# Kernel optimization log

Hardware: AMD Instinct MI355X
Metric: run time of the kernel (lower is better)

## Reference

```python
import jax, jax.numpy as jnp
import numpy as np

BETA = 0.25

def _l2norm(x, eps=1e-12):
    # F.normalize(x, dim=-1)
    n = jnp.sqrt(jnp.sum(x * x, axis=-1, keepdims=True))
    return x / jnp.maximum(n, eps)

def setup_inputs() -> dict:
    key = jax.random.key(0)
    k1, k2 = jax.random.split(key)
    z = jax.random.normal(k1, (32, 1024, 32), dtype=jnp.float32)
    embedding = jax.random.normal(k2, (8192, 32), dtype=jnp.float32)
    return {"z": z, "embedding": embedding}

def reference(z, embedding):
    B, T, D = z.shape
    zf = _l2norm(z.reshape(-1, D))            # [N, D]
    en = _l2norm(embedding)                   # [n_e, D]
    # squared distances: ||z||^2 + ||e||^2 - 2 z.e  -> [N, n_e]
    d = (jnp.sum(zf * zf, axis=1, keepdims=True)
         + jnp.sum(en * en, axis=1)
         - 2.0 * jnp.einsum('nd,kd->nk', zf, en))
    idx = jnp.argmin(d, axis=1).reshape(B, T)            # [B, T]
    z_q = embedding[idx]                                  # [B, T, D] gather
    z_qnorm = _l2norm(z_q)
    z_norm = _l2norm(z)
    loss = (BETA * jnp.mean((jax.lax.stop_gradient(z_qnorm) - z_norm) ** 2)
            + jnp.mean((z_qnorm - jax.lax.stop_gradient(z_norm)) ** 2))
    # straight-through estimator
    z_q_out = z + jax.lax.stop_gradient(z_qnorm - z)
    return z_q_out, loss, idx
```

## Files before the change

kernel.cpp:

```cpp
#include <hip/hip_runtime.h>
#include <math.h>


#define D 32
#define KCODES 8192
#define MARGIN 2.5e-4f
#define EPS 1e-12f

typedef short bf16x8 __attribute__((ext_vector_type(8)));
typedef unsigned short u16x8 __attribute__((ext_vector_type(8)));
typedef float f32x4 __attribute__((ext_vector_type(4)));

static __device__ __forceinline__ unsigned short f2bf(float x) {
  unsigned u = __float_as_uint(x);
  return (unsigned short)((u + 0x7FFFu + ((u >> 16) & 1u)) >> 16);
}
static __device__ __forceinline__ float bf2f(unsigned short s) {
  return __uint_as_float(((unsigned)s) << 16);
}
static __device__ __forceinline__ void gload_lds16(const void* g, void* l) {
  __builtin_amdgcn_global_load_lds(
      (const __attribute__((address_space(1))) void*)g,
      (__attribute__((address_space(3))) void*)l, 16, 0, 0);
}


__global__ __launch_bounds__(256) void k_prep(const float* __restrict__ z,
                                              const float* __restrict__ emb,
                                              float* __restrict__ en,
                                              float* __restrict__ en_h,
                                              unsigned short* __restrict__ eswz,
                                              unsigned short* __restrict__ zswz_hi,
                                              unsigned short* __restrict__ zswz_lo,
                                              float* __restrict__ zn,
                                              int* __restrict__ cnt,
                                              float* __restrict__ loss,
                                              unsigned long long* __restrict__ mp2,
                                              int N) {
  int v = blockIdx.x * 256 + threadIdx.x;
  if (v == 0) { *cnt = 0; *loss = 0.f; }
  if (v >= KCODES + N) return;
  if (v >= KCODES) mp2[v - KCODES] = 0ull;
  const float* src = (v < KCODES) ? (emb + (size_t)v * D) : (z + (size_t)(v - KCODES) * D);

  float x[D];
  const float4* p = reinterpret_cast<const float4*>(src);
#pragma unroll
  for (int j = 0; j < D / 4; ++j) {
    float4 q = p[j];
    x[4 * j + 0] = q.x; x[4 * j + 1] = q.y; x[4 * j + 2] = q.z; x[4 * j + 3] = q.w;
  }
  float ss = 0.f;
#pragma unroll
  for (int j = 0; j < D; ++j) ss = fmaf(x[j], x[j], ss);
  float n = fmaxf(sqrtf(ss), EPS);
#pragma unroll
  for (int j = 0; j < D; ++j) x[j] = x[j] / n;

  unsigned short hi[D], lo[D];
#pragma unroll
  for (int j = 0; j < D; ++j) {
    hi[j] = f2bf(x[j]);
    lo[j] = f2bf(x[j] - bf2f(hi[j]));
  }

  if (v < KCODES) {
    float4* o = reinterpret_cast<float4*>(en + (size_t)v * D);
    float s2 = 0.f;
#pragma unroll
    for (int j = 0; j < D / 4; ++j) {
      float4 q = {x[4 * j], x[4 * j + 1], x[4 * j + 2], x[4 * j + 3]};
      s2 = fmaf(q.x, q.x, fmaf(q.y, q.y, fmaf(q.z, q.z, fmaf(q.w, q.w, s2))));
      o[j] = q;
    }
    en_h[v] = 0.5f * s2;
    int tl = v >> 4, m = v & 15;
#pragma unroll
    for (int q = 0; q < 4; ++q) {
      u16x8 hv, lv;
#pragma unroll
      for (int j = 0; j < 8; ++j) { hv[j] = hi[8 * q + j]; lv[j] = lo[8 * q + j]; }
      *(u16x8*)(eswz + (size_t)tl * 1024 + (q * 16 + m) * 8) = hv;
      *(u16x8*)(eswz + (size_t)tl * 1024 + 512 + (q * 16 + m) * 8) = lv;
    }
  } else {
    int r = v - KCODES;
    float4* zo = reinterpret_cast<float4*>(zn + (size_t)r * D);
#pragma unroll
    for (int j = 0; j < D / 4; ++j) {
      float4 q = {x[4 * j], x[4 * j + 1], x[4 * j + 2], x[4 * j + 3]};
      zo[j] = q;
    }
    int g = r >> 4, m = r & 15;
#pragma unroll
    for (int q = 0; q < 4; ++q) {
      u16x8 hv, lv;
#pragma unroll
      for (int j = 0; j < 8; ++j) { hv[j] = hi[8 * q + j]; lv[j] = lo[8 * q + j]; }
      *(u16x8*)(zswz_hi + (size_t)g * 512 + (q * 16 + m) * 8) = hv;
      *(u16x8*)(zswz_lo + (size_t)g * 512 + (q * 16 + m) * 8) = lv;
    }
  }
}

__global__ __launch_bounds__(256, 2) void k_argmin_mfma(
    const unsigned short* __restrict__ zswz_hi,
    const unsigned short* __restrict__ zswz_lo,
    const unsigned short* __restrict__ eswz,
    float* __restrict__ res_s1, int* __restrict__ res_cb,
    float* __restrict__ res_s2) {
  __shared__ unsigned short lds_sh[2][16384];

  const int tid = threadIdx.x;
  const int wid = tid >> 6, lane = tid & 63;
  const int lane15 = lane & 15, quad = lane >> 4;
  const int rs = blockIdx.x >> 2;
  const int qt = blockIdx.x & 3;

  bf16x8 zhi[4], zlo[4];
#pragma unroll
  for (int rg = 0; rg < 4; ++rg) {
    int g = rs * 16 + wid * 4 + rg;
    zhi[rg] = *(const bf16x8*)(zswz_hi + (size_t)g * 512 + lane * 8);
    zlo[rg] = *(const bf16x8*)(zswz_lo + (size_t)g * 512 + lane * 8);
  }

  float cm[4], s1g[4], s2c[4];
  int cb[4];
#pragma unroll
  for (int rg = 0; rg < 4; ++rg) {
    cm[rg] = -3.4e38f; s1g[rg] = -3.4e38f; s2c[rg] = -3.4e38f; cb[rg] = 0;
  }
  const f32x4 zero4 = {0.f, 0.f, 0.f, 0.f};

  const float4* gall = reinterpret_cast<const float4*>(eswz) + (size_t)qt * 8 * 2048;
#pragma unroll
  for (int i = 0; i < 8; ++i) {
    int off = i * 256 + tid;
    gload_lds16(gall + off, (char*)&lds_sh[0][0] + (size_t)off * 16);
  }

  for (int c = 0; c < 8; ++c) {
    __syncthreads();
    if (c + 1 < 8) {
      const float4* gn = gall + (size_t)(c + 1) * 2048;
      char* dst = (char*)&lds_sh[(c + 1) & 1][0];
#pragma unroll
      for (int i = 0; i < 8; ++i) {
        int off = i * 256 + tid;
        gload_lds16(gn + off, dst + (size_t)off * 16);
      }
    }
    const unsigned short* buf = &lds_sh[c & 1][0];
#pragma unroll
    for (int t = 0; t < 16; ++t) {
      bf16x8 ahi = *(const bf16x8*)(buf + t * 1024 + lane * 8);
      bf16x8 alo = *(const bf16x8*)(buf + t * 1024 + 512 + lane * 8);
#pragma unroll
      for (int rg = 0; rg < 4; ++rg) {
        f32x4 acc = __builtin_amdgcn_mfma_f32_16x16x32_bf16(ahi, zhi[rg], zero4, 0, 0, 0);
        acc = __builtin_amdgcn_mfma_f32_16x16x32_bf16(ahi, zlo[rg], acc, 0, 0, 0);
        acc = __builtin_amdgcn_mfma_f32_16x16x32_bf16(alo, zhi[rg], acc, 0, 0, 0);
        cm[rg] = fmaxf(cm[rg],
                       fmaxf(fmaxf(acc[0], acc[1]), fmaxf(acc[2], acc[3])));
      }
    }
#pragma unroll
    for (int rg = 0; rg < 4; ++rg) {
      float old1 = s1g[rg];
      s2c[rg] = fmaxf(s2c[rg], fminf(cm[rg], old1));
      bool better = cm[rg] > old1;
      cb[rg] = better ? (qt * 8 + c) : cb[rg];
      s1g[rg] = better ? cm[rg] : old1;
      cm[rg] = -3.4e38f;
    }
  }

#pragma unroll
  for (int m = 16; m <= 32; m <<= 1) {
#pragma unroll
    for (int rg = 0; rg < 4; ++rg) {
      float o1 = __shfl_xor(s1g[rg], m, 64);
      float o2 = __shfl_xor(s2c[rg], m, 64);
      int ob = __shfl_xor(cb[rg], m, 64);
      s2c[rg] = fmaxf(fmaxf(s2c[rg], o2), fminf(s1g[rg], o1));
      bool better = o1 > s1g[rg];
      s1g[rg] = better ? o1 : s1g[rg];
      cb[rg] = better ? ob : cb[rg];
    }
  }
  if (quad == 0) {
#pragma unroll
    for (int rg = 0; rg < 4; ++rg) {
      int row = rs * 256 + wid * 64 + rg * 16 + lane15;
      res_s1[(size_t)row * 4 + qt] = s1g[rg];
      res_cb[(size_t)row * 4 + qt] = cb[rg];
      res_s2[(size_t)row * 4 + qt] = s2c[rg];
    }
  }
}

__global__ __launch_bounds__(256) void k_merge(const float* __restrict__ res_s1,
                                               const int* __restrict__ res_cb,
                                               const float* __restrict__ res_s2,
                                               int* __restrict__ row_cb,
                                               float* __restrict__ row_s2) {
  int row = blockIdx.x * 256 + threadIdx.x;
  float4 s1q = reinterpret_cast<const float4*>(res_s1)[row];
  float4 s2q = reinterpret_cast<const float4*>(res_s2)[row];
  int4 cbq = reinterpret_cast<const int4*>(res_cb)[row];
  float s1b = s1q.x;  int cbb = cbq.x;  float s2b = s2q.x;
  {
    float s1p = s1q.y, s2p = s2q.y; int cbp = cbq.y;
    s2b = fmaxf(fmaxf(s2b, s2p), fminf(s1b, s1p));
    bool better = s1p > s1b;  s1b = better ? s1p : s1b;  cbb = better ? cbp : cbb;
  }
  {
    float s1p = s1q.z, s2p = s2q.z; int cbp = cbq.z;
    s2b = fmaxf(fmaxf(s2b, s2p), fminf(s1b, s1p));
    bool better = s1p > s1b;  s1b = better ? s1p : s1b;  cbb = better ? cbp : cbb;
  }
  {
    float s1p = s1q.w, s2p = s2q.w; int cbp = cbq.w;
    s2b = fmaxf(fmaxf(s2b, s2p), fminf(s1b, s1p));
    bool better = s1p > s1b;  s1b = better ? s1p : s1b;  cbb = better ? cbp : cbb;
  }
  row_cb[row] = cbb;
  row_s2[row] = s2b;
}

__global__ __launch_bounds__(256) void k_rescore(
    const float* __restrict__ zn, const float* __restrict__ en,
    const float* __restrict__ en_h,
    const int* __restrict__ row_cb, const float* __restrict__ row_s2,
    int* __restrict__ idx_ws, int* __restrict__ list, int* __restrict__ cnt,
    int N) {
  __shared__ float en_s[256 * 36];
  __shared__ float enh_s[256];
  __shared__ unsigned short rows_s[2048];
  __shared__ int nmatch;

  const int tid = threadIdx.x;
  const int c = blockIdx.x >> 4;
  const int sb = blockIdx.x & 15;
  const int rows_per = N >> 4;
  const int r0 = sb * rows_per;

  if (tid == 0) nmatch = 0;
  const float4* e4 = reinterpret_cast<const float4*>(en) + (size_t)c * 2048;
#pragma unroll
  for (int i = 0; i < 8; ++i) {
    int idx = i * 256 + tid;
    float4 v4 = e4[idx];
    int code = idx >> 3, j = idx & 7;
    *reinterpret_cast<float4*>(&en_s[code * 36 + j * 4]) = v4;
  }
  enh_s[tid] = en_h[c * 256 + tid];
  __syncthreads();

  for (int i = 0; i < rows_per / 256; ++i) {
    int rrel = i * 256 + tid;
    if (row_cb[r0 + rrel] == c) {
      int pos = atomicAdd(&nmatch, 1);
      rows_s[pos] = (unsigned short)rrel;
    }
  }
  __syncthreads();
  const int nm = nmatch;
  const int lane = tid & 63, wid = tid >> 6;

  for (int ri = wid; ri < nm; ri += 4) {
    int row = __builtin_amdgcn_readfirstlane(r0 + (int)rows_s[ri]);
    const float* znr = zn + (size_t)row * D;
    float v[D];
#pragma unroll
    for (int d = 0; d < D; ++d) v[d] = znr[d];

    unsigned long long best = 0ull;
#pragma unroll
    for (int cc = 0; cc < 4; ++cc) {
      int kl = lane + cc * 64;
      float a = -enh_s[kl];
      const float* ep = &en_s[kl * 36];
#pragma unroll
      for (int jj = 0; jj < 8; ++jj) {
        float4 e = *reinterpret_cast<const float4*>(&ep[jj * 4]);
        a = fmaf(v[4 * jj + 0], e.x, a);
        a = fmaf(v[4 * jj + 1], e.y, a);
        a = fmaf(v[4 * jj + 2], e.z, a);
        a = fmaf(v[4 * jj + 3], e.w, a);
      }
      int k = c * 256 + kl;
      unsigned o = __float_as_uint(a);
      o = (o & 0x80000000u) ? ~o : (o | 0x80000000u);
      unsigned long long pk = ((unsigned long long)o << 32) | (unsigned)(8191 - k);
      best = (pk > best) ? pk : best;
    }
#pragma unroll
    for (int m = 32; m >= 1; m >>= 1) {
      unsigned long long op = __shfl_xor(best, m, 64);
      best = (op > best) ? op : best;
    }
    if (lane == 0) {
      unsigned uo = (unsigned)(best >> 32);
      unsigned uu = (uo & 0x80000000u) ? (uo & 0x7FFFFFFFu) : ~uo;
      float sC = __uint_as_float(uu);
      int kC = 8191 - (int)(unsigned)(best & 0xFFFFFFFFull);
      float dotw = sC + enh_s[kC - c * 256];
      if (row_s2[row] > dotw - MARGIN) {
        int pos = atomicAdd(cnt, 1);
        list[pos] = row;
        idx_ws[row] = -(pos + 1);
      } else {
        idx_ws[row] = kC;
      }
    }
  }
}

__global__ __launch_bounds__(256) void k_cleanup(const float* __restrict__ zn,
                                                 const float* __restrict__ en,
                                                 const float* __restrict__ en_h,
                                                 const int* __restrict__ list,
                                                 const int* __restrict__ cnt,
                                                 unsigned long long* __restrict__ mp2) {
  __shared__ unsigned long long wred[4];
  const int tid = threadIdx.x;
  const int lane = tid & 63, wid = tid >> 6;
  const int ntask = (*cnt) * 32;

  for (int j = blockIdx.x; j < ntask; j += gridDim.x) {
    int i = j >> 5, kc = j & 31;
    int row = list[i];
    const float* znr = zn + (size_t)row * D;
    float v[D];
#pragma unroll
    for (int d = 0; d < D; ++d) v[d] = znr[d];

    int k = kc * 256 + tid;
    const float4* er = reinterpret_cast<const float4*>(en + (size_t)k * D);
    float a = -en_h[k];
#pragma unroll
    for (int jj = 0; jj < 8; ++jj) {
      float4 e = er[jj];
      a = fmaf(v[4 * jj + 0], e.x, a);
      a = fmaf(v[4 * jj + 1], e.y, a);
      a = fmaf(v[4 * jj + 2], e.z, a);
      a = fmaf(v[4 * jj + 3], e.w, a);
    }
    unsigned o = __float_as_uint(a);
    o = (o & 0x80000000u) ? ~o : (o | 0x80000000u);
    unsigned long long pk = ((unsigned long long)o << 32) | (unsigned)(8191 - k);
#pragma unroll
    for (int m = 32; m >= 1; m >>= 1) {
      unsigned long long op = __shfl_xor(pk, m, 64);
      pk = (op > pk) ? op : pk;
    }
    if (lane == 0) wred[wid] = pk;
    __syncthreads();
    if (tid == 0) {
      unsigned long long m01 = (wred[0] > wred[1]) ? wred[0] : wred[1];
      unsigned long long m23 = (wred[2] > wred[3]) ? wred[2] : wred[3];
      atomicMax(&mp2[i], (m01 > m23) ? m01 : m23);
    }
    __syncthreads();
  }
}

__global__ __launch_bounds__(256) void k_epi(const float* __restrict__ z,
                                             const float* __restrict__ en,
                                             const int* __restrict__ idx_ws,
                                             const unsigned long long* __restrict__ mp2,
                                             float* __restrict__ out_z,
                                             float* __restrict__ loss,
                                             float* __restrict__ out_idx,
                                             float scale) {
  int row = blockIdx.x * 256 + threadIdx.x;
  int kb = idx_ws[row];
  if (kb < 0) {
    unsigned long long m = mp2[-kb - 1];
    kb = 8191 - (int)(unsigned)(m & 0xFFFFFFFFull);
  }
  out_idx[row] = (float)kb;

  const float4* p = reinterpret_cast<const float4*>(z + (size_t)row * D);
  float4 q[D / 4];
#pragma unroll
  for (int j = 0; j < D / 4; ++j) q[j] = p[j];
  float ss = 0.f;
#pragma unroll
  for (int j = 0; j < D / 4; ++j)
    ss = fmaf(q[j].x, q[j].x, fmaf(q[j].y, q[j].y, fmaf(q[j].z, q[j].z, fmaf(q[j].w, q[j].w, ss))));
  float n = fmaxf(sqrtf(ss), EPS);

  const float4* ep = reinterpret_cast<const float4*>(en + (size_t)kb * D);
  float4* op = reinterpret_cast<float4*>(out_z + (size_t)row * D);
  float s = 0.f;
#pragma unroll
  for (int j = 0; j < D / 4; ++j) {
    float4 e = ep[j];
    float4 o;
    o.x = q[j].x + (e.x - q[j].x);
    o.y = q[j].y + (e.y - q[j].y);
    o.z = q[j].z + (e.z - q[j].z);
    o.w = q[j].w + (e.w - q[j].w);
    op[j] = o;
    float dx = e.x - q[j].x / n;  float dy = e.y - q[j].y / n;
    float dz = e.z - q[j].z / n;  float dw = e.w - q[j].w / n;
    s = fmaf(dx, dx, fmaf(dy, dy, fmaf(dz, dz, fmaf(dw, dw, s))));
  }

#pragma unroll
  for (int off = 32; off > 0; off >>= 1) s += __shfl_down(s, off, 64);
  __shared__ float wsum[4];
  int lane = threadIdx.x & 63, wid = threadIdx.x >> 6;
  if (lane == 0) wsum[wid] = s;
  __syncthreads();
  if (threadIdx.x == 0) {
    float tt = (wsum[0] + wsum[1]) + (wsum[2] + wsum[3]);
    atomicAdd(loss, tt * scale);
  }
}

extern "C" void kernel_launch(void* const* d_in, const int* in_sizes, int n_in,
                              void* d_out, int out_size, void* d_ws, size_t ws_size,
                              hipStream_t stream) {
  const float* z = (const float*)d_in[0];
  const float* emb = (const float*)d_in[1];
  const int N = in_sizes[0] / D;
  const int K = in_sizes[1] / D;

  float* out = (float*)d_out;
  float* out_z = out;
  float* loss = out + (size_t)N * D;
  float* out_idx = out + (size_t)N * D + 1;

  float* zn = out_z;

  char* w = (char*)d_ws;
  float* en = (float*)w;                         w += (size_t)K * D * 4;
  float* en_h = (float*)w;                       w += (size_t)K * 4;
  unsigned short* eswz = (unsigned short*)w;     w += (size_t)K * D * 2 * 2;
  unsigned short* zswz_hi = (unsigned short*)w;  w += (size_t)N * D * 2;
  unsigned short* zswz_lo = (unsigned short*)w;  w += (size_t)N * D * 2;
  int* idx_ws = (int*)w;                         w += (size_t)N * 4;
  int* list = (int*)w;                           w += (size_t)N * 4;
  unsigned long long* mp2 = (unsigned long long*)w; w += (size_t)N * 8;
  float* res_s1 = (float*)w;                     w += (size_t)N * 4 * 4;
  int* res_cb = (int*)w;                         w += (size_t)N * 4 * 4;
  float* res_s2 = (float*)w;                     w += (size_t)N * 4 * 4;
  int* row_cb = (int*)w;                         w += (size_t)N * 4;
  float* row_s2 = (float*)w;                     w += (size_t)N * 4;
  int* cnt = (int*)w;

  k_prep<<<dim3((K + N) / 256), 256, 0, stream>>>(
      z, emb, en, en_h, eswz, zswz_hi, zswz_lo, zn, cnt, loss, mp2, N);

  k_argmin_mfma<<<dim3((N / 256) * 4), 256, 0, stream>>>(
      zswz_hi, zswz_lo, eswz, res_s1, res_cb, res_s2);

  k_merge<<<dim3(N / 256), 256, 0, stream>>>(
      res_s1, res_cb, res_s2, row_cb, row_s2);

  k_rescore<<<dim3(32 * 16), 256, 0, stream>>>(
      zn, en, en_h, row_cb, row_s2, idx_ws, list, cnt, N);

  k_cleanup<<<dim3(4096), 256, 0, stream>>>(zn, en, en_h, list, cnt, mp2);

  k_epi<<<dim3(N / 256), 256, 0, stream>>>(
      z, en, idx_ws, mp2, out_z, loss, out_idx, 1.25f / (float)((size_t)N * D));
}
```

Before: 172.8 us.

## Halve argmin chunk size and fold full-codebook fallback into rescore kernel

The MFMA argmin pass now uses 128-code chunks (16 per block instead of 8) with half the LDS and a higher occupancy hint, so the coarse candidate chunk is narrower. The rescore kernel covers 128-code chunks and, for rows flagged ambiguous, runs the full exhaustive search in-block and writes the index directly. This removes the separate cleanup kernel, the global atomic list and the mp2 packed-max buffer. The aim is to cut rescore work and one launch, at the risk of serial per-block fallback loops if many rows get flagged.

```diff
diff --git a/kernel.cpp b/kernel.cpp
--- a/kernel.cpp
+++ b/kernel.cpp
@@ -4,6 +4,8 @@
 
 #define D 32
 #define KCODES 8192
+#define CH 128
+#define NCHUNK (KCODES / CH)
 #define MARGIN 2.5e-4f
 #define EPS 1e-12f
 
@@ -33,14 +35,11 @@
                                               unsigned short* __restrict__ zswz_hi,
                                               unsigned short* __restrict__ zswz_lo,
                                               float* __restrict__ zn,
-                                              int* __restrict__ cnt,
                                               float* __restrict__ loss,
-                                              unsigned long long* __restrict__ mp2,
                                               int N) {
   int v = blockIdx.x * 256 + threadIdx.x;
-  if (v == 0) { *cnt = 0; *loss = 0.f; }
+  if (v == 0) *loss = 0.f;
   if (v >= KCODES + N) return;
-  if (v >= KCODES) mp2[v - KCODES] = 0ull;
   const float* src = (v < KCODES) ? (emb + (size_t)v * D) : (z + (size_t)(v - KCODES) * D);
 
   float x[D];
@@ -103,13 +102,13 @@
   }
 }
 
-__global__ __launch_bounds__(256, 2) void k_argmin_mfma(
+__global__ __launch_bounds__(256, 4) void k_argmin_mfma(
     const unsigned short* __restrict__ zswz_hi,
     const unsigned short* __restrict__ zswz_lo,
     const unsigned short* __restrict__ eswz,
     float* __restrict__ res_s1, int* __restrict__ res_cb,
     float* __restrict__ res_s2) {
-  __shared__ unsigned short lds_sh[2][16384];
+  __shared__ unsigned short lds_sh[2][8192];
 
   const int tid = threadIdx.x;
   const int wid = tid >> 6, lane = tid & 63;
@@ -133,27 +132,27 @@
   }
   const f32x4 zero4 = {0.f, 0.f, 0.f, 0.f};
 
-  const float4* gall = reinterpret_cast<const float4*>(eswz) + (size_t)qt * 8 * 2048;
-#pragma unroll
-  for (int i = 0; i < 8; ++i) {
+  const float4* gall = reinterpret_cast<const float4*>(eswz) + (size_t)qt * 16 * 1024;
+#pragma unroll
+  for (int i = 0; i < 4; ++i) {
     int off = i * 256 + tid;
     gload_lds16(gall + off, (char*)&lds_sh[0][0] + (size_t)off * 16);
   }
 
-  for (int c = 0; c < 8; ++c) {
+  for (int c = 0; c < 16; ++c) {
     __syncthreads();
-    if (c + 1 < 8) {
-      const float4* gn = gall + (size_t)(c + 1) * 2048;
+    if (c + 1 < 16) {
+      const float4* gn = gall + (size_t)(c + 1) * 1024;
       char* dst = (char*)&lds_sh[(c + 1) & 1][0];
 #pragma unroll
-      for (int i = 0; i < 8; ++i) {
+      for (int i = 0; i < 4; ++i) {
         int off = i * 256 + tid;
         gload_lds16(gn + off, dst + (size_t)off * 16);
       }
     }
     const unsigned short* buf = &lds_sh[c & 1][0];
 #pragma unroll
-    for (int t = 0; t < 16; ++t) {
+    for (int t = 0; t < 8; ++t) {
       bf16x8 ahi = *(const bf16x8*)(buf + t * 1024 + lane * 8);
       bf16x8 alo = *(const bf16x8*)(buf + t * 1024 + 512 + lane * 8);
 #pragma unroll
@@ -170,7 +169,7 @@
       float old1 = s1g[rg];
       s2c[rg] = fmaxf(s2c[rg], fminf(cm[rg], old1));
       bool better = cm[rg] > old1;
-      cb[rg] = better ? (qt * 8 + c) : cb[rg];
+      cb[rg] = better ? (qt * 16 + c) : cb[rg];
       s1g[rg] = better ? cm[rg] : old1;
       cm[rg] = -3.4e38f;
     }
@@ -233,29 +232,30 @@
     const float* __restrict__ zn, const float* __restrict__ en,
     const float* __restrict__ en_h,
     const int* __restrict__ row_cb, const float* __restrict__ row_s2,
-    int* __restrict__ idx_ws, int* __restrict__ list, int* __restrict__ cnt,
-    int N) {
-  __shared__ float en_s[256 * 36];
-  __shared__ float enh_s[256];
-  __shared__ unsigned short rows_s[2048];
-  __shared__ int nmatch;
+    int* __restrict__ idx_ws, int N) {
+  __shared__ float en_s[CH * 36];
+  __shared__ float enh_s[CH];
+  __shared__ unsigned short rows_s[4096];
+  __shared__ unsigned short flg_s[4096];
+  __shared__ unsigned long long wred[4];
+  __shared__ int nmatch, nflag;
 
   const int tid = threadIdx.x;
-  const int c = blockIdx.x >> 4;
-  const int sb = blockIdx.x & 15;
-  const int rows_per = N >> 4;
+  const int c = blockIdx.x >> 3;
+  const int sb = blockIdx.x & 7;
+  const int rows_per = N >> 3;
   const int r0 = sb * rows_per;
 
-  if (tid == 0) nmatch = 0;
-  const float4* e4 = reinterpret_cast<const float4*>(en) + (size_t)c * 2048;
-#pragma unroll
-  for (int i = 0; i < 8; ++i) {
+  if (tid == 0) { nmatch = 0; nflag = 0; }
+  const float4* e4 = reinterpret_cast<const float4*>(en) + (size_t)c * (CH * 8);
+#pragma unroll
+  for (int i = 0; i < 4; ++i) {
     int idx = i * 256 + tid;
     float4 v4 = e4[idx];
     int code = idx >> 3, j = idx & 7;
     *reinterpret_cast<float4*>(&en_s[code * 36 + j * 4]) = v4;
   }
-  enh_s[tid] = en_h[c * 256 + tid];
+  if (tid < CH) enh_s[tid] = en_h[c * CH + tid];
   __syncthreads();
 
   for (int i = 0; i < rows_per / 256; ++i) {
@@ -270,7 +270,8 @@
   const int lane = tid & 63, wid = tid >> 6;
 
   for (int ri = wid; ri < nm; ri += 4) {
-    int row = __builtin_amdgcn_readfirstlane(r0 + (int)rows_s[ri]);
+    int rrel = (int)rows_s[ri];
+    int row = __builtin_amdgcn_readfirstlane(r0 + rrel);
     const float* znr = zn + (size_t)row * D;
     float v[D];
 #pragma unroll
@@ -278,7 +279,7 @@
 
     unsigned long long best = 0ull;
 #pragma unroll
-    for (int cc = 0; cc < 4; ++cc) {
+    for (int cc = 0; cc < CH / 64; ++cc) {
       int kl = lane + cc * 64;
       float a = -enh_s[kl];
       const float* ep = &en_s[kl * 36];
@@ -290,7 +291,7 @@
         a = fmaf(v[4 * jj + 2], e.z, a);
         a = fmaf(v[4 * jj + 3], e.w, a);
       }
-      int k = c * 256 + kl;
+      int k = c * CH + kl;
       unsigned o = __float_as_uint(a);
       o = (o & 0x80000000u) ? ~o : (o | 0x80000000u);
       unsigned long long pk = ((unsigned long long)o << 32) | (unsigned)(8191 - k);
@@ -306,62 +307,56 @@
       unsigned uu = (uo & 0x80000000u) ? (uo & 0x7FFFFFFFu) : ~uo;
       float sC = __uint_as_float(uu);
       int kC = 8191 - (int)(unsigned)(best & 0xFFFFFFFFull);
-      float dotw = sC + enh_s[kC - c * 256];
+      float dotw = sC + enh_s[kC - c * CH];
       if (row_s2[row] > dotw - MARGIN) {
-        int pos = atomicAdd(cnt, 1);
-        list[pos] = row;
-        idx_ws[row] = -(pos + 1);
+        int pos = atomicAdd(&nflag, 1);
+        flg_s[pos] = (unsigned short)rrel;
       } else {
         idx_ws[row] = kC;
       }
     }
   }
-}
-
-__global__ __launch_bounds__(256) void k_cleanup(const float* __restrict__ zn,
-                                                 const float* __restrict__ en,
-                                                 const float* __restrict__ en_h,
-                                                 const int* __restrict__ list,
-                                                 const int* __restrict__ cnt,
-                                                 unsigned long long* __restrict__ mp2) {
-  __shared__ unsigned long long wred[4];
-  const int tid = threadIdx.x;
-  const int lane = tid & 63, wid = tid >> 6;
-  const int ntask = (*cnt) * 32;
-
-  for (int j = blockIdx.x; j < ntask; j += gridDim.x) {
-    int i = j >> 5, kc = j & 31;
-    int row = list[i];
+  __syncthreads();
+  const int nf = nflag;
+
+  for (int fi = 0; fi < nf; ++fi) {
+    int row = __builtin_amdgcn_readfirstlane(r0 + (int)flg_s[fi]);
     const float* znr = zn + (size_t)row * D;
     float v[D];
 #pragma unroll
     for (int d = 0; d < D; ++d) v[d] = znr[d];
 
-    int k = kc * 256 + tid;
-    const float4* er = reinterpret_cast<const float4*>(en + (size_t)k * D);
-    float a = -en_h[k];
-#pragma unroll
-    for (int jj = 0; jj < 8; ++jj) {
-      float4 e = er[jj];
-      a = fmaf(v[4 * jj + 0], e.x, a);
-      a = fmaf(v[4 * jj + 1], e.y, a);
-      a = fmaf(v[4 * jj + 2], e.z, a);
-      a = fmaf(v[4 * jj + 3], e.w, a);
-    }
-    unsigned o = __float_as_uint(a);
-    o = (o & 0x80000000u) ? ~o : (o | 0x80000000u);
-    unsigned long long pk = ((unsigned long long)o << 32) | (unsigned)(8191 - k);
+    unsigned long long best = 0ull;
+#pragma unroll
+    for (int cc = 0; cc < 32; ++cc) {
+      int k = wid * 2048 + cc * 64 + lane;
+      const float4* er = reinterpret_cast<const float4*>(en + (size_t)k * D);
+      float a = -en_h[k];
+#pragma unroll
+      for (int jj = 0; jj < 8; ++jj) {
+        float4 e = er[jj];
+        a = fmaf(v[4 * jj + 0], e.x, a);
+        a = fmaf(v[4 * jj + 1], e.y, a);
+        a = fmaf(v[4 * jj + 2], e.z, a);
+        a = fmaf(v[4 * jj + 3], e.w, a);
+      }
+      unsigned o = __float_as_uint(a);
+      o = (o & 0x80000000u) ? ~o : (o | 0x80000000u);
+      unsigned long long pk = ((unsigned long long)o << 32) | (unsigned)(8191 - k);
+      best = (pk > best) ? pk : best;
+    }
 #pragma unroll
     for (int m = 32; m >= 1; m >>= 1) {
-      unsigned long long op = __shfl_xor(pk, m, 64);
-      pk = (op > pk) ? op : pk;
-    }
-    if (lane == 0) wred[wid] = pk;
+      unsigned long long op = __shfl_xor(best, m, 64);
+      best = (op > best) ? op : best;
+    }
+    if (lane == 0) wred[wid] = best;
     __syncthreads();
     if (tid == 0) {
       unsigned long long m01 = (wred[0] > wred[1]) ? wred[0] : wred[1];
       unsigned long long m23 = (wred[2] > wred[3]) ? wred[2] : wred[3];
-      atomicMax(&mp2[i], (m01 > m23) ? m01 : m23);
+      unsigned long long mm = (m01 > m23) ? m01 : m23;
+      idx_ws[row] = 8191 - (int)(unsigned)(mm & 0xFFFFFFFFull);
     }
     __syncthreads();
   }
@@ -370,17 +365,12 @@
 __global__ __launch_bounds__(256) void k_epi(const float* __restrict__ z,
                                              const float* __restrict__ en,
                                              const int* __restrict__ idx_ws,
-                                             const unsigned long long* __restrict__ mp2,
                                              float* __restrict__ out_z,
                                              float* __restrict__ loss,
                                              float* __restrict__ out_idx,
                                              float scale) {
   int row = blockIdx.x * 256 + threadIdx.x;
   int kb = idx_ws[row];
-  if (kb < 0) {
-    unsigned long long m = mp2[-kb - 1];
-    kb = 8191 - (int)(unsigned)(m & 0xFFFFFFFFull);
-  }
   out_idx[row] = (float)kb;
 
   const float4* p = reinterpret_cast<const float4*>(z + (size_t)row * D);
@@ -444,17 +434,14 @@
   unsigned short* zswz_hi = (unsigned short*)w;  w += (size_t)N * D * 2;
   unsigned short* zswz_lo = (unsigned short*)w;  w += (size_t)N * D * 2;
   int* idx_ws = (int*)w;                         w += (size_t)N * 4;
-  int* list = (int*)w;                           w += (size_t)N * 4;
-  unsigned long long* mp2 = (unsigned long long*)w; w += (size_t)N * 8;
   float* res_s1 = (float*)w;                     w += (size_t)N * 4 * 4;
   int* res_cb = (int*)w;                         w += (size_t)N * 4 * 4;
   float* res_s2 = (float*)w;                     w += (size_t)N * 4 * 4;
   int* row_cb = (int*)w;                         w += (size_t)N * 4;
   float* row_s2 = (float*)w;                     w += (size_t)N * 4;
-  int* cnt = (int*)w;
 
   k_prep<<<dim3((K + N) / 256), 256, 0, stream>>>(
-      z, emb, en, en_h, eswz, zswz_hi, zswz_lo, zn, cnt, loss, mp2, N);
+      z, emb, en, en_h, eswz, zswz_hi, zswz_lo, zn, loss, N);
 
   k_argmin_mfma<<<dim3((N / 256) * 4), 256, 0, stream>>>(
       zswz_hi, zswz_lo, eswz, res_s1, res_cb, res_s2);
@@ -462,11 +449,9 @@
   k_merge<<<dim3(N / 256), 256, 0, stream>>>(
       res_s1, res_cb, res_s2, row_cb, row_s2);
 
-  k_rescore<<<dim3(32 * 16), 256, 0, stream>>>(
-      zn, en, en_h, row_cb, row_s2, idx_ws, list, cnt, N);
-
-  k_cleanup<<<dim3(4096), 256, 0, stream>>>(zn, en, en_h, list, cnt, mp2);
+  k_rescore<<<dim3(NCHUNK * 8), 256, 0, stream>>>(
+      zn, en, en_h, row_cb, row_s2, idx_ws, N);
 
   k_epi<<<dim3(N / 256), 256, 0, stream>>>(
-      z, en, idx_ws, mp2, out_z, loss, out_idx, 1.25f / (float)((size_t)N * D));
-}
+      z, en, idx_ws, out_z, loss, out_idx, 1.25f / (float)((size_t)N * D));
+}
```

New measurement: 445.0 us. 2.58x slower.
